# Kernel optimization log

Hardware: AMD Instinct MI355X
Metric: run time of the kernel (lower is better)

The kernel has to match this reference:

```python
import jax, jax.numpy as jnp
import numpy as np
from math import sqrt

HEAD_DIM = 128
MASKED = True


def setup_inputs() -> dict:
    key = jax.random.key(0)
    kq, kk, kv = jax.random.split(key, 3)
    B, S, D = 16, 2048, HEAD_DIM
    return {
        "queries": jax.random.normal(kq, (B, S, D), dtype=jnp.float32),
        "keys": jax.random.normal(kk, (B, S, D), dtype=jnp.float32),
        "values": jax.random.normal(kv, (B, S, D), dtype=jnp.float32),
    }


def reference(queries, keys, values):
    # scores: (B, Sq, Sk)
    scores = jnp.einsum("bqd,bkd->bqk", queries, keys) / sqrt(HEAD_DIM)
    if MASKED:
        # Faithful to torch.tril: upper-triangular entries set to 0.0
        # (NOT -inf) BEFORE softmax — reproduces the original's
        # multiplicative mask semantics exactly.
        scores = jnp.tril(scores)
    weights = jax.nn.softmax(scores, axis=-1)
    return jnp.einsum("bqk,bkd->bqd", weights, values)
```

## Files before the change

kernel.cpp:

```cpp
#include <hip/hip_runtime.h>
#include <hip/hip_bf16.h>

#define DEVI static __device__ __forceinline__

typedef __attribute__((ext_vector_type(8))) short short8;
typedef __attribute__((ext_vector_type(16))) float f32x16;
typedef __attribute__((ext_vector_type(2))) unsigned int uintx2;

#define S_LEN 2048
#define D_DIM 128
#define NBATCH 16
#define QSC ((float)(0.08838834764831845 * 1.4426950408889634))
#define MFIX 8.0f
#define E8 0.00390625f

#if __has_builtin(__builtin_amdgcn_exp2f)
#define EXP2(x) __builtin_amdgcn_exp2f(x)
#else
#define EXP2(x) exp2f(x)
#endif

DEVI unsigned short f2bf(float x) {
  union { float f; unsigned int u; } a; a.f = x;
  unsigned int u = a.u;
  unsigned int r = (u + 0x7fffu + ((u >> 16) & 1u)) >> 16;
  return (unsigned short)r;
}

DEVI unsigned int cvtpk(float lo, float hi) {
  unsigned int r;
  asm volatile("v_cvt_pk_bf16_f32 %0, %1, %2" : "=v"(r) : "v"(lo), "v"(hi));
  return r;
}

DEVI void plswap(unsigned int& a, unsigned int& b) {
  uintx2 r = __builtin_amdgcn_permlane32_swap(a, b, false, false);
  a = r[0];
  b = r[1];
}

DEVI float xhalf_sum(float x) {
  union { float f; unsigned int u; } a, b;
  a.f = x; b.f = x;
  plswap(a.u, b.u);
  return a.f + b.f;
}


__global__ void prep(const float* __restrict__ K, const float* __restrict__ V,
                     unsigned short* __restrict__ Kb, unsigned short* __restrict__ Vt,
                     float* __restrict__ Tsum) {
  __shared__ unsigned short t[64][68];
  const int tt = threadIdx.x;
  if (blockIdx.x >= 1024) {
    const int M4 = (NBATCH * S_LEN * D_DIM) / 4;
    for (int i = (blockIdx.x - 1024) * 256 + tt; i < M4; i += 2048 * 256) {
      const size_t idx = (size_t)i * 4;
      const float4 v = *reinterpret_cast<const float4*>(K + idx);
      ushort4 o;
      o.x = f2bf(v.x); o.y = f2bf(v.y); o.z = f2bf(v.z); o.w = f2bf(v.w);
      *reinterpret_cast<ushort4*>(Kb + idx) = o;
    }
    return;
  }
  const int bid = blockIdx.x;
  const int b = bid >> 6, rem = bid & 63;
  const int st = rem & 31, s0 = st * 64, d0 = (rem >> 5) * 64;
  const int r = tt >> 2, c = (tt & 3) * 16;
  const float* src = V + ((size_t)(b * S_LEN + s0 + r)) * D_DIM + d0 + c;
#pragma unroll
  for (int i = 0; i < 4; i++) {
    float4 v = reinterpret_cast<const float4*>(src)[i];
    t[r][c + 4 * i + 0] = f2bf(v.x);
    t[r][c + 4 * i + 1] = f2bf(v.y);
    t[r][c + 4 * i + 2] = f2bf(v.z);
    t[r][c + 4 * i + 3] = f2bf(v.w);
  }
  __syncthreads();
  unsigned short* dst = Vt + (((size_t)(b * 32 + st)) * 128 + d0 + r) * 64 + c;
#pragma unroll
  for (int i = 0; i < 4; i++) {
    ushort4 o;
    o.x = t[c + 4 * i + 0][r];
    o.y = t[c + 4 * i + 1][r];
    o.z = t[c + 4 * i + 2][r];
    o.w = t[c + 4 * i + 3][r];
    reinterpret_cast<ushort4*>(dst)[i] = o;
  }
  if (tt < 64) {
    float s = 0.0f;
#pragma unroll 8
    for (int rr = 0; rr < 64; rr++) {
      union { float f; unsigned int u; } cv;
      cv.u = ((unsigned int)t[rr][tt]) << 16;
      s += cv.f;
    }
    Tsum[((size_t)b * 32 + st) * 128 + d0 + tt] = s;
  }
}

__global__ void sufB(const float* __restrict__ Tsum, float* __restrict__ SufV) {
  const int b = blockIdx.x;
  const int d = threadIdx.x;
  float v[32];
#pragma unroll
  for (int t = 0; t < 32; t++) v[t] = Tsum[((size_t)b * 32 + t) * 128 + d];
  float run = 0.0f;
  SufV[((size_t)b * 33 + 32) * 128 + d] = 0.0f;
#pragma unroll
  for (int t = 31; t >= 0; t--) {
    run += v[t];
    SufV[((size_t)b * 33 + t) * 128 + d] = run;
  }
}


#define AS1 __attribute__((address_space(1)))
#define AS3 __attribute__((address_space(3)))

DEVI short8 ldK(const char* ldsK, int row, int off) {
  int addr = row * 256 + (off ^ ((row & 15) << 4));
  return *reinterpret_cast<const short8*>(ldsK + addr);
}
DEVI short8 ldV(const char* ldsV, int row, int off) {
  int addr = row * 128 + (off ^ ((row & 7) << 4));
  return *reinterpret_cast<const short8*>(ldsV + addr);
}

template <bool MASK>
DEVI void tile_body(const char* cb, const short8* qf, f32x16 (&acc)[4],
                    float& l_run, const int ln31, const int h, const int kh,
                    const int qrow, const int kvb) {
  f32x16 sT;
#pragma unroll
  for (int r = 0; r < 16; r++) sT[r] = 0.0f;
  __builtin_amdgcn_s_setprio(1);
#pragma unroll
  for (int kf = 0; kf < 8; kf++) {
    short8 af = ldK(cb, ln31 + 32 * kh, 32 * kf + 16 * h);
    sT = __builtin_amdgcn_mfma_f32_32x32x16_bf16(af, qf[kf], sT, 0, 0, 0);
  }
  __builtin_amdgcn_s_setprio(0);
  if (MASK) {
#pragma unroll
    for (int r = 0; r < 16; r++) {
      int kvg = kvb + (r & 3) + 8 * (r >> 2) + 4 * h;
      if (kvg > qrow) sT[r] = 0.0f;
    }
  }
#pragma unroll
  for (int r = 0; r < 16; r++) sT[r] = EXP2(sT[r] - MFIX);
  float ts[8];
#pragma unroll
  for (int r = 0; r < 8; r++) ts[r] = sT[r] + sT[r + 8];
#pragma unroll
  for (int r = 0; r < 4; r++) ts[r] = ts[r] + ts[r + 4];
  float sum = (ts[0] + ts[1]) + (ts[2] + ts[3]);
  sum = xhalf_sum(sum);
  l_run += sum;
#pragma unroll
  for (int kl = 0; kl < 2; kl++) {
    const int ra = 8 * kl;
    const int rb = 8 * kl + 4;
    unsigned int a0 = cvtpk(sT[ra + 0], sT[ra + 1]);
    unsigned int a1 = cvtpk(sT[ra + 2], sT[ra + 3]);
    unsigned int b0 = cvtpk(sT[rb + 0], sT[rb + 1]);
    unsigned int b1 = cvtpk(sT[rb + 2], sT[rb + 3]);
    plswap(a0, b0);
    plswap(a1, b1);
    union { short8 v; unsigned int u[4]; } pa;
    pa.u[0] = a0; pa.u[1] = a1; pa.u[2] = b0; pa.u[3] = b1;
    const int vboff = 64 * kh + 32 * kl + 16 * h;
    __builtin_amdgcn_s_setprio(1);
#pragma unroll
    for (int nt = 0; nt < 4; nt++) {
      short8 vb = ldV(cb + 16384, ln31 + 32 * nt, vboff);
      acc[nt] = __builtin_amdgcn_mfma_f32_32x32x16_bf16(pa.v, vb, acc[nt], 0, 0, 0);
    }
    __builtin_amdgcn_s_setprio(0);
  }
}

#define SMEM_BYTES 32768

__global__ __launch_bounds__(256, 2) void attn_kernel(
    const float* __restrict__ Q, const unsigned short* __restrict__ Kb,
    const unsigned short* __restrict__ Vt, const float* __restrict__ SufV,
    float* __restrict__ out) {
  __shared__ __align__(16) char smem[SMEM_BYTES];

  const int tid = threadIdx.x;
  const int w = tid >> 6, lane = tid & 63;
  const int ln31 = lane & 31, h = lane >> 5;
  const int kh = w & 1;
  const int qh = w >> 1;

  const int bid = blockIdx.x;
  const int x = bid & 7, idx = bid >> 3;
  const int b = 2 * x + (idx & 1);
  const int j = 31 - (idx >> 1);

  const int q0 = j * 64;
  const int kv_end = q0 + 64;
  const int qrow = q0 + 32 * qh + ln31;

  int off[8];
  const char* tbase;
  int dstpart;
  if (w < 2) {
#pragma unroll
    for (int i = 0; i < 8; i++) {
      int L = (w * 8 + i) * 1024 + lane * 16;
      int row = L >> 8;
      off[i] = row * 256 + ((L & 255) ^ ((row & 15) << 4));
    }
    tbase = (const char*)(Kb + (size_t)b * S_LEN * D_DIM);
    dstpart = w * 8192;
  } else {
#pragma unroll
    for (int i = 0; i < 8; i++) {
      int L = ((w - 2) * 8 + i) * 1024 + lane * 16;
      int row = L >> 7;
      off[i] = (L & ~127) + ((L & 127) ^ ((row & 7) << 4));
    }
    tbase = (const char*)Vt + (size_t)b * (S_LEN * D_DIM * 2);
    dstpart = 16384 + (w - 2) * 8192;
  }

#define STAGE(t)                                                               \
  do {                                                                         \
    const char* src_ = tbase + (size_t)(t) * 16384;                            \
    _Pragma("unroll")                                                          \
    for (int i = 0; i < 8; i++) {                                              \
      __builtin_amdgcn_global_load_lds((const AS1 unsigned int*)(src_ + off[i]),\
                                       (AS3 unsigned int*)(smem + dstpart + i * 1024),\
                                       16, 0, 0);                              \
    }                                                                          \
  } while (0)

  short8 qf[8];
  {
    const float* qsrc = Q + ((size_t)b * S_LEN + qrow) * D_DIM + 8 * h;
#pragma unroll
    for (int kf = 0; kf < 8; kf++) {
      float4 a = *reinterpret_cast<const float4*>(qsrc + 16 * kf);
      float4 d = *reinterpret_cast<const float4*>(qsrc + 16 * kf + 4);
      union { short8 v; unsigned int u[4]; } q8;
      q8.u[0] = cvtpk(a.x * QSC, a.y * QSC);
      q8.u[1] = cvtpk(a.z * QSC, a.w * QSC);
      q8.u[2] = cvtpk(d.x * QSC, d.y * QSC);
      q8.u[3] = cvtpk(d.z * QSC, d.w * QSC);
      qf[kf] = q8.v;
    }
  }

  f32x16 acc[4];
#pragma unroll
  for (int nt = 0; nt < 4; nt++)
#pragma unroll
    for (int rr = 0; rr < 16; rr++) acc[nt][rr] = 0.0f;
  float l_run = 0.0f;

  for (int kt = 0; kt <= j; kt++) {
    STAGE(kt);
    __syncthreads();
    if (kt < j)
      tile_body<false>(smem, qf, acc, l_run, ln31, h, kh, qrow,
                       kt * 64 + 32 * kh);
    else
      tile_body<true>(smem, qf, acc, l_run, ln31, h, kh, qrow,
                      kt * 64 + 32 * kh);
    __syncthreads();
  }

  float* lsh = (float*)smem;
  if (kh == 1 && h == 0) lsh[qh * 32 + ln31] = l_run;
  __syncthreads();
  float l_other = lsh[qh * 32 + ln31];
  __syncthreads();
  float* pbase = (float*)smem + qh * 4096;
  if (kh == 1) {
#pragma unroll
    for (int nt = 0; nt < 4; nt++)
#pragma unroll
      for (int rr = 0; rr < 16; rr++) {
        int cr = (rr & 3) + 8 * (rr >> 2) + 4 * h;
        pbase[cr * 128 + ln31 + 32 * nt] = acc[nt][rr];
      }
  }
  __syncthreads();
  if (kh == 0) {
    float l_tot = l_run + l_other + (float)(S_LEN - kv_end) * E8;
    const float* sv = SufV + ((size_t)b * 33 + (kv_end >> 6)) * 128;
    float* ob = out + ((size_t)b * S_LEN + q0 + 32 * qh) * D_DIM + ln31;
#pragma unroll
    for (int nt = 0; nt < 4; nt++) {
      float svv = sv[ln31 + 32 * nt];
#pragma unroll
      for (int rr = 0; rr < 16; rr++) {
        int cr = (rr & 3) + 8 * (rr >> 2) + 4 * h;
        float v = acc[nt][rr] + pbase[cr * 128 + ln31 + 32 * nt] + E8 * svv;
        float lq = __shfl(l_tot, cr);
        ob[(size_t)cr * D_DIM + 32 * nt] = v / lq;
      }
    }
  }
}


extern "C" void kernel_launch(void* const* d_in, const int* in_sizes, int n_in,
                              void* d_out, int out_size, void* d_ws, size_t ws_size,
                              hipStream_t stream) {
  const float* Q = (const float*)d_in[0];
  const float* K = (const float*)d_in[1];
  const float* V = (const float*)d_in[2];
  float* out = (float*)d_out;

  char* ws = (char*)d_ws;
  unsigned short* Kb = (unsigned short*)ws;
  unsigned short* Vt = Kb + 4194304;
  float* Tsum = (float*)(ws + 16777216);
  float* SufV = Tsum + 65536;

  prep<<<3072, 256, 0, stream>>>(K, V, Kb, Vt, Tsum);
  sufB<<<16, 128, 0, stream>>>(Tsum, SufV);
  attn_kernel<<<512, 256, 0, stream>>>(Q, Kb, Vt, SufV, out);
}
```

Baseline: 66.20 us.

## Load K/V fragments directly from global memory, pair causal strips per block

The attention kernel no longer stages K and V tiles into LDS. Each wave now loads its MFMA fragments straight from global memory, which removes the per-tile __syncthreads barriers. Blocks double to 512 threads: two wave groups take alternating KV tiles, and their partial accumulators are reduced through a larger LDS area. Each block processes one long and one short causal strip (j=31-p and j=p) to balance load, and the grid is halved. The costs are uncoalesced, lower-reuse global loads, heavier register pressure, and a bigger LDS footprint that may reduce occupancy.

```diff
diff --git a/kernel.cpp b/kernel.cpp
--- a/kernel.cpp
+++ b/kernel.cpp
@@ -115,32 +115,30 @@
 }
 
 
-#define AS1 __attribute__((address_space(1)))
-#define AS3 __attribute__((address_space(3)))
-
-DEVI short8 ldK(const char* ldsK, int row, int off) {
-  int addr = row * 256 + (off ^ ((row & 15) << 4));
-  return *reinterpret_cast<const short8*>(ldsK + addr);
-}
-DEVI short8 ldV(const char* ldsV, int row, int off) {
-  int addr = row * 128 + (off ^ ((row & 7) << 4));
-  return *reinterpret_cast<const short8*>(ldsV + addr);
-}
-
 template <bool MASK>
-DEVI void tile_body(const char* cb, const short8* qf, f32x16 (&acc)[4],
-                    float& l_run, const int ln31, const int h, const int kh,
-                    const int qrow, const int kvb) {
+DEVI void tile_body(const char* kt, const char* vt, const int krowoff,
+                    const int vrowoff, const short8* qf, f32x16 (&acc)[4],
+                    float& l_run, const int h, const int kh, const int qrow,
+                    const int kvb) {
+  short8 kfr[8];
+#pragma unroll
+  for (int kf = 0; kf < 8; kf++)
+    kfr[kf] = *reinterpret_cast<const short8*>(kt + krowoff + 32 * kf);
   f32x16 sT;
 #pragma unroll
   for (int r = 0; r < 16; r++) sT[r] = 0.0f;
   __builtin_amdgcn_s_setprio(1);
 #pragma unroll
-  for (int kf = 0; kf < 8; kf++) {
-    short8 af = ldK(cb, ln31 + 32 * kh, 32 * kf + 16 * h);
-    sT = __builtin_amdgcn_mfma_f32_32x32x16_bf16(af, qf[kf], sT, 0, 0, 0);
-  }
+  for (int kf = 0; kf < 8; kf++)
+    sT = __builtin_amdgcn_mfma_f32_32x32x16_bf16(kfr[kf], qf[kf], sT, 0, 0, 0);
   __builtin_amdgcn_s_setprio(0);
+  short8 vfr[8];
+#pragma unroll
+  for (int kl = 0; kl < 2; kl++)
+#pragma unroll
+    for (int nt = 0; nt < 4; nt++)
+      vfr[kl * 4 + nt] = *reinterpret_cast<const short8*>(
+          vt + vrowoff + 32 * kl + 4096 * nt);
   if (MASK) {
 #pragma unroll
     for (int r = 0; r < 16; r++) {
@@ -170,73 +168,25 @@
     plswap(a1, b1);
     union { short8 v; unsigned int u[4]; } pa;
     pa.u[0] = a0; pa.u[1] = a1; pa.u[2] = b0; pa.u[3] = b1;
-    const int vboff = 64 * kh + 32 * kl + 16 * h;
     __builtin_amdgcn_s_setprio(1);
 #pragma unroll
-    for (int nt = 0; nt < 4; nt++) {
-      short8 vb = ldV(cb + 16384, ln31 + 32 * nt, vboff);
-      acc[nt] = __builtin_amdgcn_mfma_f32_32x32x16_bf16(pa.v, vb, acc[nt], 0, 0, 0);
-    }
+    for (int nt = 0; nt < 4; nt++)
+      acc[nt] = __builtin_amdgcn_mfma_f32_32x32x16_bf16(pa.v, vfr[kl * 4 + nt],
+                                                        acc[nt], 0, 0, 0);
     __builtin_amdgcn_s_setprio(0);
   }
 }
 
-#define SMEM_BYTES 32768
-
-__global__ __launch_bounds__(256, 2) void attn_kernel(
-    const float* __restrict__ Q, const unsigned short* __restrict__ Kb,
-    const unsigned short* __restrict__ Vt, const float* __restrict__ SufV,
-    float* __restrict__ out) {
-  __shared__ __align__(16) char smem[SMEM_BYTES];
-
-  const int tid = threadIdx.x;
-  const int w = tid >> 6, lane = tid & 63;
-  const int ln31 = lane & 31, h = lane >> 5;
-  const int kh = w & 1;
-  const int qh = w >> 1;
-
-  const int bid = blockIdx.x;
-  const int x = bid & 7, idx = bid >> 3;
-  const int b = 2 * x + (idx & 1);
-  const int j = 31 - (idx >> 1);
-
+#define SMEM_BYTES 99328
+
+DEVI void run_strip(int j, int b, char* smem, const float* __restrict__ Q,
+                    const char* kbB, const char* vbB,
+                    const float* __restrict__ SufV, float* __restrict__ out,
+                    int qs, int kh, int grp, int ln31, int h) {
   const int q0 = j * 64;
   const int kv_end = q0 + 64;
-  const int qrow = q0 + 32 * qh + ln31;
-
-  int off[8];
-  const char* tbase;
-  int dstpart;
-  if (w < 2) {
-#pragma unroll
-    for (int i = 0; i < 8; i++) {
-      int L = (w * 8 + i) * 1024 + lane * 16;
-      int row = L >> 8;
-      off[i] = row * 256 + ((L & 255) ^ ((row & 15) << 4));
-    }
-    tbase = (const char*)(Kb + (size_t)b * S_LEN * D_DIM);
-    dstpart = w * 8192;
-  } else {
-#pragma unroll
-    for (int i = 0; i < 8; i++) {
-      int L = ((w - 2) * 8 + i) * 1024 + lane * 16;
-      int row = L >> 7;
-      off[i] = (L & ~127) + ((L & 127) ^ ((row & 7) << 4));
-    }
-    tbase = (const char*)Vt + (size_t)b * (S_LEN * D_DIM * 2);
-    dstpart = 16384 + (w - 2) * 8192;
-  }
-
-#define STAGE(t)                                                               \
-  do {                                                                         \
-    const char* src_ = tbase + (size_t)(t) * 16384;                            \
-    _Pragma("unroll")                                                          \
-    for (int i = 0; i < 8; i++) {                                              \
-      __builtin_amdgcn_global_load_lds((const AS1 unsigned int*)(src_ + off[i]),\
-                                       (AS3 unsigned int*)(smem + dstpart + i * 1024),\
-                                       16, 0, 0);                              \
-    }                                                                          \
-  } while (0)
+  const int qrow = q0 + 32 * qs + ln31;
+  const int pidx = kh * 2 + grp;
 
   short8 qf[8];
   {
@@ -261,50 +211,80 @@
     for (int rr = 0; rr < 16; rr++) acc[nt][rr] = 0.0f;
   float l_run = 0.0f;
 
-  for (int kt = 0; kt <= j; kt++) {
-    STAGE(kt);
-    __syncthreads();
-    if (kt < j)
-      tile_body<false>(smem, qf, acc, l_run, ln31, h, kh, qrow,
-                       kt * 64 + 32 * kh);
+  const int krowoff = (ln31 + 32 * kh) * 256 + 16 * h;
+  const int vrowoff = ln31 * 128 + 64 * kh + 16 * h;
+
+  for (int t = grp; t <= j; t += 2) {
+    const char* kt = kbB + (size_t)t * 16384;
+    const char* vt = vbB + (size_t)t * 16384;
+    if (t == j)
+      tile_body<true>(kt, vt, krowoff, vrowoff, qf, acc, l_run, h, kh, qrow,
+                      t * 64 + 32 * kh);
     else
-      tile_body<true>(smem, qf, acc, l_run, ln31, h, kh, qrow,
-                      kt * 64 + 32 * kh);
-    __syncthreads();
-  }
-
-  float* lsh = (float*)smem;
-  if (kh == 1 && h == 0) lsh[qh * 32 + ln31] = l_run;
-  __syncthreads();
-  float l_other = lsh[qh * 32 + ln31];
-  __syncthreads();
-  float* pbase = (float*)smem + qh * 4096;
-  if (kh == 1) {
+      tile_body<false>(kt, vt, krowoff, vrowoff, qf, acc, l_run, h, kh, qrow,
+                       t * 64 + 32 * kh);
+  }
+
+  float* lsh = (float*)(smem + 98304);
+  if (pidx != 0) {
+    float* reg = (float*)smem + (qs * 3 + pidx - 1) * 4096;
 #pragma unroll
     for (int nt = 0; nt < 4; nt++)
 #pragma unroll
       for (int rr = 0; rr < 16; rr++) {
         int cr = (rr & 3) + 8 * (rr >> 2) + 4 * h;
-        pbase[cr * 128 + ln31 + 32 * nt] = acc[nt][rr];
+        reg[cr * 128 + ln31 + 32 * nt] = acc[nt][rr];
       }
+    if (h == 0) lsh[(qs * 3 + pidx - 1) * 32 + ln31] = l_run;
   }
   __syncthreads();
-  if (kh == 0) {
-    float l_tot = l_run + l_other + (float)(S_LEN - kv_end) * E8;
+  if (pidx == 0) {
+    float l_tot = l_run + lsh[(qs * 3 + 0) * 32 + ln31] +
+                  lsh[(qs * 3 + 1) * 32 + ln31] + lsh[(qs * 3 + 2) * 32 + ln31] +
+                  (float)(S_LEN - kv_end) * E8;
     const float* sv = SufV + ((size_t)b * 33 + (kv_end >> 6)) * 128;
-    float* ob = out + ((size_t)b * S_LEN + q0 + 32 * qh) * D_DIM + ln31;
+    const float* r0 = (float*)smem + (qs * 3 + 0) * 4096;
+    const float* r1 = (float*)smem + (qs * 3 + 1) * 4096;
+    const float* r2 = (float*)smem + (qs * 3 + 2) * 4096;
+    float* ob = out + ((size_t)b * S_LEN + q0 + 32 * qs) * D_DIM + ln31;
 #pragma unroll
     for (int nt = 0; nt < 4; nt++) {
       float svv = sv[ln31 + 32 * nt];
 #pragma unroll
       for (int rr = 0; rr < 16; rr++) {
         int cr = (rr & 3) + 8 * (rr >> 2) + 4 * h;
-        float v = acc[nt][rr] + pbase[cr * 128 + ln31 + 32 * nt] + E8 * svv;
-        float lq = __shfl(l_tot, cr);
-        ob[(size_t)cr * D_DIM + 32 * nt] = v / lq;
+        int cidx = cr * 128 + ln31 + 32 * nt;
+        float v = acc[nt][rr] + r0[cidx] + r1[cidx] + r2[cidx] + E8 * svv;
+        ob[(size_t)cr * D_DIM + 32 * nt] = v / __shfl(l_tot, cr);
       }
     }
   }
+  __syncthreads();
+}
+
+__global__ __launch_bounds__(512, 2) void attn_kernel(
+    const float* __restrict__ Q, const unsigned short* __restrict__ Kb,
+    const unsigned short* __restrict__ Vt, const float* __restrict__ SufV,
+    float* __restrict__ out) {
+  __shared__ __align__(16) char smem[SMEM_BYTES];
+
+  const int tid = threadIdx.x;
+  const int w = tid >> 6, lane = tid & 63;
+  const int ln31 = lane & 31, h = lane >> 5;
+  const int qs = w >> 2;
+  const int kh = (w >> 1) & 1;
+  const int grp = w & 1;
+
+  const int bid = blockIdx.x;
+  const int x = bid & 7, idx = bid >> 3;
+  const int b = 2 * x + (idx & 1);
+  const int p = idx >> 1;
+
+  const char* kbB = (const char*)(Kb + (size_t)b * S_LEN * D_DIM);
+  const char* vbB = (const char*)Vt + (size_t)b * (S_LEN * D_DIM * 2);
+
+  run_strip(31 - p, b, smem, Q, kbB, vbB, SufV, out, qs, kh, grp, ln31, h);
+  run_strip(p, b, smem, Q, kbB, vbB, SufV, out, qs, kh, grp, ln31, h);
 }
 
 
@@ -324,5 +304,5 @@
 
   prep<<<3072, 256, 0, stream>>>(K, V, Kb, Vt, Tsum);
   sufB<<<16, 128, 0, stream>>>(Tsum, SufV);
-  attn_kernel<<<512, 256, 0, stream>>>(Q, Kb, Vt, SufV, out);
-}
+  attn_kernel<<<256, 512, 0, stream>>>(Q, Kb, Vt, SufV, out);
+}
```

New measurement: 94.66 us. +43.0%, slower.

## Use 128-row tiles with double-buffered K/V staging and per-warp causal skip

Applied to the files above, without the earlier changes.

The attention kernel now processes 128-query blocks with 512 threads. K/V tiles of 128 keys are double-buffered in LDS so the global-to-LDS load of the next tile overlaps compute on the current one. Each warp skips 32-key chunks lying fully above its causal diagonal and applies the mask only on the diagonal chunk. The V transpose layout and suffix sums move to 32-row granularity to match. This removes one barrier per iteration and hides load latency, at the cost of about 129KB of LDS per block (one block per CU) and half as many blocks.

```diff
diff --git a/kernel.cpp b/kernel.cpp
--- a/kernel.cpp
+++ b/kernel.cpp
@@ -77,7 +77,8 @@
     t[r][c + 4 * i + 3] = f2bf(v.w);
   }
   __syncthreads();
-  unsigned short* dst = Vt + (((size_t)(b * 32 + st)) * 128 + d0 + r) * 64 + c;
+  unsigned short* dst =
+      Vt + (((size_t)(b * 16 + (st >> 1))) * 128 + d0 + r) * 128 + (st & 1) * 64 + c;
 #pragma unroll
   for (int i = 0; i < 4; i++) {
     ushort4 o;
@@ -87,30 +88,31 @@
     o.w = t[c + 4 * i + 3][r];
     reinterpret_cast<ushort4*>(dst)[i] = o;
   }
-  if (tt < 64) {
+  if (tt < 128) {
+    const int half = tt >> 6, dc = tt & 63;
     float s = 0.0f;
 #pragma unroll 8
-    for (int rr = 0; rr < 64; rr++) {
+    for (int rr = 0; rr < 32; rr++) {
       union { float f; unsigned int u; } cv;
-      cv.u = ((unsigned int)t[rr][tt]) << 16;
+      cv.u = ((unsigned int)t[half * 32 + rr][dc]) << 16;
       s += cv.f;
     }
-    Tsum[((size_t)b * 32 + st) * 128 + d0 + tt] = s;
+    Tsum[((size_t)(b * 64 + st * 2 + half)) * 128 + d0 + dc] = s;
   }
 }
 
 __global__ void sufB(const float* __restrict__ Tsum, float* __restrict__ SufV) {
   const int b = blockIdx.x;
   const int d = threadIdx.x;
-  float v[32];
-#pragma unroll
-  for (int t = 0; t < 32; t++) v[t] = Tsum[((size_t)b * 32 + t) * 128 + d];
+  float v[64];
+#pragma unroll
+  for (int t = 0; t < 64; t++) v[t] = Tsum[((size_t)b * 64 + t) * 128 + d];
   float run = 0.0f;
-  SufV[((size_t)b * 33 + 32) * 128 + d] = 0.0f;
-#pragma unroll
-  for (int t = 31; t >= 0; t--) {
+  SufV[((size_t)b * 65 + 64) * 128 + d] = 0.0f;
+#pragma unroll
+  for (int t = 63; t >= 0; t--) {
     run += v[t];
-    SufV[((size_t)b * 33 + t) * 128 + d] = run;
+    SufV[((size_t)b * 65 + t) * 128 + d] = run;
   }
 }
 
@@ -118,33 +120,27 @@
 #define AS1 __attribute__((address_space(1)))
 #define AS3 __attribute__((address_space(3)))
 
-DEVI short8 ldK(const char* ldsK, int row, int off) {
-  int addr = row * 256 + (off ^ ((row & 15) << 4));
-  return *reinterpret_cast<const short8*>(ldsK + addr);
-}
-DEVI short8 ldV(const char* ldsV, int row, int off) {
-  int addr = row * 128 + (off ^ ((row & 7) << 4));
-  return *reinterpret_cast<const short8*>(ldsV + addr);
-}
-
 template <bool MASK>
-DEVI void tile_body(const char* cb, const short8* qf, f32x16 (&acc)[4],
-                    float& l_run, const int ln31, const int h, const int kh,
-                    const int qrow, const int kvb) {
+DEVI void chunk_body(const char* kb, const char* vb, const int kq,
+                     const short8* qf, f32x16 (&acc)[4], float& l_run,
+                     const int ln31, const int h, const int qrow, const int kbq) {
+  const int krow = 32 * kq + ln31;
+  const int ksw = (krow & 15) << 4;
+  const char* kbase = kb + krow * 256;
   f32x16 sT;
 #pragma unroll
   for (int r = 0; r < 16; r++) sT[r] = 0.0f;
   __builtin_amdgcn_s_setprio(1);
 #pragma unroll
   for (int kf = 0; kf < 8; kf++) {
-    short8 af = ldK(cb, ln31 + 32 * kh, 32 * kf + 16 * h);
+    short8 af = *reinterpret_cast<const short8*>(kbase + ((32 * kf + 16 * h) ^ ksw));
     sT = __builtin_amdgcn_mfma_f32_32x32x16_bf16(af, qf[kf], sT, 0, 0, 0);
   }
   __builtin_amdgcn_s_setprio(0);
   if (MASK) {
 #pragma unroll
     for (int r = 0; r < 16; r++) {
-      int kvg = kvb + (r & 3) + 8 * (r >> 2) + 4 * h;
+      int kvg = kbq + (r & 3) + 8 * (r >> 2) + 4 * h;
       if (kvg > qrow) sT[r] = 0.0f;
     }
   }
@@ -158,6 +154,7 @@
   float sum = (ts[0] + ts[1]) + (ts[2] + ts[3]);
   sum = xhalf_sum(sum);
   l_run += sum;
+  const int vsw = (ln31 & 15) << 4;
 #pragma unroll
   for (int kl = 0; kl < 2; kl++) {
     const int ra = 8 * kl;
@@ -170,20 +167,20 @@
     plswap(a1, b1);
     union { short8 v; unsigned int u[4]; } pa;
     pa.u[0] = a0; pa.u[1] = a1; pa.u[2] = b0; pa.u[3] = b1;
-    const int vboff = 64 * kh + 32 * kl + 16 * h;
+    const int vo = (64 * kq + 32 * kl + 16 * h) ^ vsw;
     __builtin_amdgcn_s_setprio(1);
 #pragma unroll
     for (int nt = 0; nt < 4; nt++) {
-      short8 vb = ldV(cb + 16384, ln31 + 32 * nt, vboff);
-      acc[nt] = __builtin_amdgcn_mfma_f32_32x32x16_bf16(pa.v, vb, acc[nt], 0, 0, 0);
+      short8 vf = *reinterpret_cast<const short8*>(vb + (ln31 + 32 * nt) * 256 + vo);
+      acc[nt] = __builtin_amdgcn_mfma_f32_32x32x16_bf16(pa.v, vf, acc[nt], 0, 0, 0);
     }
     __builtin_amdgcn_s_setprio(0);
   }
 }
 
-#define SMEM_BYTES 32768
-
-__global__ __launch_bounds__(256, 2) void attn_kernel(
+#define SMEM_BYTES 132096
+
+__global__ __launch_bounds__(512, 2) void attn_kernel(
     const float* __restrict__ Q, const unsigned short* __restrict__ Kb,
     const unsigned short* __restrict__ Vt, const float* __restrict__ SufV,
     float* __restrict__ out) {
@@ -192,49 +189,43 @@
   const int tid = threadIdx.x;
   const int w = tid >> 6, lane = tid & 63;
   const int ln31 = lane & 31, h = lane >> 5;
+  const int qq = w >> 1;
   const int kh = w & 1;
-  const int qh = w >> 1;
 
   const int bid = blockIdx.x;
-  const int x = bid & 7, idx = bid >> 3;
-  const int b = 2 * x + (idx & 1);
-  const int j = 31 - (idx >> 1);
-
-  const int q0 = j * 64;
-  const int kv_end = q0 + 64;
-  const int qrow = q0 + 32 * qh + ln31;
-
+  const int x = bid & 7, r = bid >> 3;
+  const int b = 2 * x + (r & 1);
+  const int g = 15 - (r >> 1);
+  const int q0 = g * 128;
+  const int T = g + 1;
+  const int qrow = q0 + 32 * qq + ln31;
+
+  const int part = w & 3;
   int off[8];
+#pragma unroll
+  for (int i = 0; i < 8; i++) {
+    int L = (part * 8 + i) * 1024 + lane * 16;
+    int row = L >> 8;
+    off[i] = row * 256 + ((L & 255) ^ ((row & 15) << 4));
+  }
   const char* tbase;
   int dstpart;
-  if (w < 2) {
-#pragma unroll
-    for (int i = 0; i < 8; i++) {
-      int L = (w * 8 + i) * 1024 + lane * 16;
-      int row = L >> 8;
-      off[i] = row * 256 + ((L & 255) ^ ((row & 15) << 4));
-    }
+  if (w < 4) {
     tbase = (const char*)(Kb + (size_t)b * S_LEN * D_DIM);
-    dstpart = w * 8192;
+    dstpart = part * 8192;
   } else {
-#pragma unroll
-    for (int i = 0; i < 8; i++) {
-      int L = ((w - 2) * 8 + i) * 1024 + lane * 16;
-      int row = L >> 7;
-      off[i] = (L & ~127) + ((L & 127) ^ ((row & 7) << 4));
-    }
-    tbase = (const char*)Vt + (size_t)b * (S_LEN * D_DIM * 2);
-    dstpart = 16384 + (w - 2) * 8192;
-  }
-
-#define STAGE(t)                                                               \
+    tbase = (const char*)(Vt + (size_t)b * S_LEN * D_DIM);
+    dstpart = 32768 + part * 8192;
+  }
+
+#define STAGE(t, bufb)                                                         \
   do {                                                                         \
-    const char* src_ = tbase + (size_t)(t) * 16384;                            \
+    const char* src_ = tbase + (size_t)(t) * 32768;                            \
     _Pragma("unroll")                                                          \
-    for (int i = 0; i < 8; i++) {                                              \
-      __builtin_amdgcn_global_load_lds((const AS1 unsigned int*)(src_ + off[i]),\
-                                       (AS3 unsigned int*)(smem + dstpart + i * 1024),\
-                                       16, 0, 0);                              \
+    for (int i_ = 0; i_ < 8; i_++) {                                           \
+      __builtin_amdgcn_global_load_lds(                                        \
+          (const AS1 unsigned int*)(src_ + off[i_]),                           \
+          (AS3 unsigned int*)(smem + (bufb) + dstpart + i_ * 1024), 16, 0, 0); \
     }                                                                          \
   } while (0)
 
@@ -261,24 +252,29 @@
     for (int rr = 0; rr < 16; rr++) acc[nt][rr] = 0.0f;
   float l_run = 0.0f;
 
-  for (int kt = 0; kt <= j; kt++) {
-    STAGE(kt);
+  STAGE(0, 0);
+  __syncthreads();
+  for (int t = 0; t < T; t++) {
+    const int bb = (t & 1) << 16;
+    if (t + 1 < T) STAGE(t + 1, bb ^ 65536);
+    const char* kb = smem + bb;
+    const char* vb = smem + bb + 32768;
+#pragma unroll
+    for (int c = 0; c < 2; c++) {
+      const int kq = 2 * kh + c;
+      const int kbq = 128 * t + 32 * kq;
+      if (kbq <= q0 + 32 * qq) {
+        if (kbq == q0 + 32 * qq)
+          chunk_body<true>(kb, vb, kq, qf, acc, l_run, ln31, h, qrow, kbq);
+        else
+          chunk_body<false>(kb, vb, kq, qf, acc, l_run, ln31, h, qrow, kbq);
+      }
+    }
     __syncthreads();
-    if (kt < j)
-      tile_body<false>(smem, qf, acc, l_run, ln31, h, kh, qrow,
-                       kt * 64 + 32 * kh);
-    else
-      tile_body<true>(smem, qf, acc, l_run, ln31, h, kh, qrow,
-                      kt * 64 + 32 * kh);
-    __syncthreads();
-  }
-
-  float* lsh = (float*)smem;
-  if (kh == 1 && h == 0) lsh[qh * 32 + ln31] = l_run;
-  __syncthreads();
-  float l_other = lsh[qh * 32 + ln31];
-  __syncthreads();
-  float* pbase = (float*)smem + qh * 4096;
+  }
+
+  float* pbase = (float*)smem + qq * 4096;
+  float* lsh = (float*)(smem + 131072);
   if (kh == 1) {
 #pragma unroll
     for (int nt = 0; nt < 4; nt++)
@@ -287,12 +283,14 @@
         int cr = (rr & 3) + 8 * (rr >> 2) + 4 * h;
         pbase[cr * 128 + ln31 + 32 * nt] = acc[nt][rr];
       }
+    if (h == 0) lsh[qq * 32 + ln31] = l_run;
   }
   __syncthreads();
   if (kh == 0) {
-    float l_tot = l_run + l_other + (float)(S_LEN - kv_end) * E8;
-    const float* sv = SufV + ((size_t)b * 33 + (kv_end >> 6)) * 128;
-    float* ob = out + ((size_t)b * S_LEN + q0 + 32 * qh) * D_DIM + ln31;
+    const int end_w = q0 + 32 * qq + 32;
+    float l_tot = l_run + lsh[qq * 32 + ln31] + (float)(S_LEN - end_w) * E8;
+    const float* sv = SufV + ((size_t)b * 65 + (end_w >> 5)) * 128;
+    float* ob = out + ((size_t)b * S_LEN + q0 + 32 * qq) * D_DIM + ln31;
 #pragma unroll
     for (int nt = 0; nt < 4; nt++) {
       float svv = sv[ln31 + 32 * nt];
@@ -320,9 +318,9 @@
   unsigned short* Kb = (unsigned short*)ws;
   unsigned short* Vt = Kb + 4194304;
   float* Tsum = (float*)(ws + 16777216);
-  float* SufV = Tsum + 65536;
+  float* SufV = Tsum + 131072;
 
   prep<<<3072, 256, 0, stream>>>(K, V, Kb, Vt, Tsum);
   sufB<<<16, 128, 0, stream>>>(Tsum, SufV);
-  attn_kernel<<<512, 256, 0, stream>>>(Q, Kb, Vt, SufV, out);
-}
+  attn_kernel<<<256, 512, 0, stream>>>(Q, Kb, Vt, SufV, out);
+}
```

After: 59.46 us. 10.2% less time.
